# Kernel optimization log

Measured on AMD Instinct MI355X. Metric: run time of the kernel, lower is better.

The kernel has to match this reference:

```python
import jax, jax.numpy as jnp
import numpy as np

D = 1024      # hidden_size
H = 16        # num_heads
HD = D // H   # head_dim = 64
FF = 4096     # intermediate_size
DEPTH = 2
S = 2048      # packed sequence length
NSEG = 4     # number of image segments
EPS = 1e-6


def setup_inputs() -> dict:
    key = jax.random.key(0)
    ks = jax.random.split(key, 8)
    hidden_states = jax.random.normal(ks[0], (S, D), jnp.float32)
    cu_seqlens = jnp.arange(NSEG + 1, dtype=jnp.int32) * (S // NSEG)
    # rotary embedding like RiceRotaryEmbedding(head_dim//2): freqs of dim HD//4
    # per spatial axis, h/w concatenated -> HD//2, then duplicated -> HD
    inv_freq = 1.0 / (10000.0 ** (jnp.arange(0, HD // 2, 2, dtype=jnp.float32) / (HD // 2)))
    pos = jnp.arange(S, dtype=jnp.float32)
    freqs = jnp.outer(pos, inv_freq)                       # [S, HD//4]
    emb = jnp.concatenate([freqs] * 4, axis=-1)            # [S, HD]
    cos, sin = jnp.cos(emb), jnp.sin(emb)

    def w(k, shape, fan):
        return jax.random.normal(k, shape, jnp.float32) / np.sqrt(fan)

    return {
        "hidden_states": hidden_states,
        "cu_seqlens": cu_seqlens,
        "cos": cos,
        "sin": sin,
        "ln1_g": jnp.ones((DEPTH, D), jnp.float32),
        "ln1_b": jnp.zeros((DEPTH, D), jnp.float32),
        "qkv_w": w(ks[1], (DEPTH, D, 3 * D), D),
        "qkv_b": jnp.zeros((DEPTH, 3 * D), jnp.float32),
        "proj_w": w(ks[2], (DEPTH, D, D), D),
        "proj_b": jnp.zeros((DEPTH, D), jnp.float32),
        "ln2_g": jnp.ones((DEPTH, D), jnp.float32),
        "ln2_b": jnp.zeros((DEPTH, D), jnp.float32),
        "fc1_w": w(ks[3], (DEPTH, D, FF), D),
        "fc1_b": jnp.zeros((DEPTH, FF), jnp.float32),
        "fc2_w": w(ks[4], (DEPTH, FF, D), FF),
        "fc2_b": jnp.zeros((DEPTH, D), jnp.float32),
    }


def _ln(x, g, b):
    m = jnp.mean(x, axis=-1, keepdims=True)
    v = jnp.mean(jnp.square(x - m), axis=-1, keepdims=True)
    return (x - m) / jnp.sqrt(v + EPS) * g + b


def _rotate_half(x):
    x1, x2 = jnp.split(x, 2, axis=-1)
    return jnp.concatenate([-x2, x1], axis=-1)


def reference(hidden_states, cu_seqlens, cos, sin,
              ln1_g, ln1_b, qkv_w, qkv_b, proj_w, proj_b,
              ln2_g, ln2_b, fc1_w, fc1_b, fc2_w, fc2_b):
    S_, D_ = hidden_states.shape
    # segment id per token from cu_seqlens -> block-diagonal additive mask
    seg = jnp.searchsorted(cu_seqlens[1:], jnp.arange(S_, dtype=jnp.int32), side="right")
    neg = jnp.finfo(jnp.float32).min
    bias = jnp.where(seg[:, None] == seg[None, :], 0.0, neg)   # [S, S]
    cos_e = cos[:, None, :]  # broadcast over heads, [S,1,HD]
    sin_e = sin[:, None, :]
    scale = 1.0 / np.sqrt(HD)

    x = hidden_states
    for i in range(DEPTH):
        # --- attention ---
        h = _ln(x, ln1_g[i], ln1_b[i])
        qkv = h @ qkv_w[i] + qkv_b[i]                           # [S, 3D]
        q, k, v = [t.reshape(S_, H, HD) for t in jnp.split(qkv, 3, axis=-1)]
        q = q * cos_e + _rotate_half(q) * sin_e
        k = k * cos_e + _rotate_half(k) * sin_e
        scores = jnp.einsum("shd,thd->hst", q, k) * scale + bias  # [H,S,S]
        w_ = jax.nn.softmax(scores.astype(jnp.float32), axis=-1)
        ao = jnp.einsum("hst,thd->shd", w_, v).reshape(S_, D_)
        x = x + ao @ proj_w[i] + proj_b[i]
        # --- mlp ---
        h2 = _ln(x, ln2_g[i], ln2_b[i])
        x = x + jax.nn.gelu(h2 @ fc1_w[i] + fc1_b[i], approximate=False) @ fc2_w[i] + fc2_b[i]
    return x
```

## Files before the change

### kernel.cpp

```cpp
#include <hip/hip_runtime.h>
#include <hip/hip_bf16.h>
#include <math.h>

#define Dm 1024
#define Hn 16
#define HDm 64
#define FFm 4096
#define Sn 2048
#define SEG 512
#define EPSV 1e-6f

typedef __attribute__((ext_vector_type(4))) float f32x4;
typedef __attribute__((ext_vector_type(8))) short s16x8;
typedef __attribute__((ext_vector_type(4))) short s16x4;

__device__ inline short f2bf(float f) {
  __hip_bfloat16 h = __float2bfloat16(f);
  short s;
  __builtin_memcpy(&s, &h, 2);
  return s;
}
__device__ inline float bf2f(short s) {
  unsigned u = ((unsigned)(unsigned short)s) << 16;
  float f;
  __builtin_memcpy(&f, &u, 4);
  return f;
}

__device__ inline float wred_sum(float v) {
#pragma unroll
  for (int m = 32; m > 0; m >>= 1) v += __shfl_xor(v, m, 64);
  return v;
}

__device__ inline void gld16(const short* g, short* lds_base) {
  __builtin_amdgcn_global_load_lds(
      (const __attribute__((address_space(1))) void*)g,
      (__attribute__((address_space(3))) void*)lds_base, 16, 0, 0);
}

__global__ __launch_bounds__(256) void ln_kernel(const float* __restrict__ x,
                                                 const float* __restrict__ g,
                                                 const float* __restrict__ b,
                                                 short* __restrict__ out) {
  const int row = blockIdx.x;
  const int tid = threadIdx.x;
  f32x4 v = *reinterpret_cast<const f32x4*>(x + (size_t)row * Dm + tid * 4);
  float s1 = v.x + v.y + v.z + v.w;
  float s2 = v.x * v.x + v.y * v.y + v.z * v.z + v.w * v.w;
  s1 = wred_sum(s1);
  s2 = wred_sum(s2);
  __shared__ float t1[4], t2[4];
  if ((tid & 63) == 0) { t1[tid >> 6] = s1; t2[tid >> 6] = s2; }
  __syncthreads();
  s1 = t1[0] + t1[1] + t1[2] + t1[3];
  s2 = t2[0] + t2[1] + t2[2] + t2[3];
  const float mean = s1 * (1.0f / Dm);
  const float var = s2 * (1.0f / Dm) - mean * mean;
  const float rstd = rsqrtf(var + EPSV);
  f32x4 gv = *reinterpret_cast<const f32x4*>(g + tid * 4);
  f32x4 bv = *reinterpret_cast<const f32x4*>(b + tid * 4);
  s16x4 o;
#pragma unroll
  for (int j = 0; j < 4; ++j)
    o[j] = f2bf((v[j] - mean) * rstd * gv[j] + bv[j]);
  *reinterpret_cast<s16x4*>(out + (size_t)row * Dm + tid * 4) = o;
}

template <int SPLIT>
__global__ __launch_bounds__(256) void redln_bf(const short* __restrict__ pb,
                                                const float* __restrict__ bias,
                                                const float* __restrict__ res,
                                                const float* __restrict__ g,
                                                const float* __restrict__ b,
                                                float* __restrict__ xout,
                                                short* __restrict__ h) {
  const int row = blockIdx.x;
  const int tid = threadIdx.x;
  const size_t idx = (size_t)row * Dm + tid * 4;
  f32x4 o = *reinterpret_cast<const f32x4*>(res + idx);
  o += *reinterpret_cast<const f32x4*>(bias + tid * 4);
#pragma unroll
  for (int s = 0; s < SPLIT; ++s) {
    s16x4 v = *reinterpret_cast<const s16x4*>(pb + (size_t)s * Sn * Dm + idx);
#pragma unroll
    for (int j = 0; j < 4; ++j) o[j] += bf2f(v[j]);
  }
  *reinterpret_cast<f32x4*>(xout + idx) = o;
  float s1 = o.x + o.y + o.z + o.w;
  float s2 = o.x * o.x + o.y * o.y + o.z * o.z + o.w * o.w;
  s1 = wred_sum(s1);
  s2 = wred_sum(s2);
  __shared__ float t1[4], t2[4];
  if ((tid & 63) == 0) { t1[tid >> 6] = s1; t2[tid >> 6] = s2; }
  __syncthreads();
  s1 = t1[0] + t1[1] + t1[2] + t1[3];
  s2 = t2[0] + t2[1] + t2[2] + t2[3];
  const float mean = s1 * (1.0f / Dm);
  const float var = s2 * (1.0f / Dm) - mean * mean;
  const float rstd = rsqrtf(var + EPSV);
  f32x4 gv = *reinterpret_cast<const f32x4*>(g + tid * 4);
  f32x4 bv = *reinterpret_cast<const f32x4*>(b + tid * 4);
  s16x4 ho;
#pragma unroll
  for (int j = 0; j < 4; ++j)
    ho[j] = f2bf((o[j] - mean) * rstd * gv[j] + bv[j]);
  *reinterpret_cast<s16x4*>(h + idx) = ho;
}

template <int SPLIT>
__global__ __launch_bounds__(256) void fcred_bf(const short* __restrict__ pb,
                                                const float* __restrict__ bias,
                                                const float* __restrict__ res,
                                                float* __restrict__ out) {
  const size_t i = ((size_t)blockIdx.x * 256 + threadIdx.x) * 4;
  f32x4 o = *reinterpret_cast<const f32x4*>(res + i);
  o += *reinterpret_cast<const f32x4*>(bias + (i & (Dm - 1)));
#pragma unroll
  for (int s = 0; s < SPLIT; ++s) {
    s16x4 v = *reinterpret_cast<const s16x4*>(pb + (size_t)s * Sn * Dm + i);
#pragma unroll
    for (int j = 0; j < 4; ++j) o[j] += bf2f(v[j]);
  }
  *reinterpret_cast<f32x4*>(out + i) = o;
}

__global__ __launch_bounds__(256) void wt_kernel(const float* __restrict__ W,
                                                 short* __restrict__ Wt,
                                                 int K, int N, int ldw) {
  __shared__ float t[32][33];
  const int n0 = blockIdx.x * 32, k0 = blockIdx.y * 32;
  const int tx = threadIdx.x & 31, ty = threadIdx.x >> 5;
#pragma unroll
  for (int r = 0; r < 32; r += 8)
    t[r + ty][tx] = W[(size_t)(k0 + r + ty) * ldw + n0 + tx];
  __syncthreads();
#pragma unroll
  for (int r = 0; r < 32; r += 8)
    Wt[(size_t)(n0 + r + ty) * K + k0 + tx] = f2bf(t[tx][r + ty]);
}

__global__ __launch_bounds__(256) void wtb_kernel(const short* __restrict__ V,
                                                  short* __restrict__ Vt,
                                                  int K, int N, int ldv) {
  __shared__ short t[32][34];
  const int n0 = blockIdx.x * 32, k0 = blockIdx.y * 32;
  const int tx = threadIdx.x & 31, ty = threadIdx.x >> 5;
#pragma unroll
  for (int r = 0; r < 32; r += 8)
    t[r + ty][tx] = V[(size_t)(k0 + r + ty) * ldv + n0 + tx];
  __syncthreads();
#pragma unroll
  for (int r = 0; r < 32; r += 8)
    Vt[(size_t)(n0 + r + ty) * K + k0 + tx] = t[tx][r + ty];
}

__global__ __launch_bounds__(256, 2) void attn_kernel(const short* __restrict__ qkvb,
                                                      const short* __restrict__ vT,
                                                      short* __restrict__ ao) {
  __shared__ short Ps[4][16][520];
  const int tid = threadIdx.x;
  const int lane = tid & 63;
  const int wave = tid >> 6;
  const int l15 = lane & 15, lg = lane >> 4;
  const int z = blockIdx.x;
  const int qblk = blockIdx.y;
  const int seg = z & 3, head = z >> 2;
  const int qrow = seg * SEG + qblk * 64 + wave * 16;

  const short* Qg = qkvb + (size_t)(qrow + l15) * 3072 + head * HDm + lg * 8;
  s16x8 qf0 = *reinterpret_cast<const s16x8*>(Qg);
  s16x8 qf1 = *reinterpret_cast<const s16x8*>(Qg + 32);

  f32x4 acc[8][4] = {};
  const short* Kg = qkvb + (size_t)(seg * SEG + l15) * 3072 + Dm + head * HDm + lg * 8;
#pragma unroll
  for (int kt = 0; kt < 8; ++kt) {
#pragma unroll
    for (int fj = 0; fj < 4; ++fj) {
      const short* kp = Kg + (size_t)(kt * 64 + fj * 16) * 3072;
      s16x8 b0 = *reinterpret_cast<const s16x8*>(kp);
      s16x8 b1 = *reinterpret_cast<const s16x8*>(kp + 32);
      acc[kt][fj] = __builtin_amdgcn_mfma_f32_16x16x32_bf16(qf0, b0, acc[kt][fj], 0, 0, 0);
      acc[kt][fj] = __builtin_amdgcn_mfma_f32_16x16x32_bf16(qf1, b1, acc[kt][fj], 0, 0, 0);
    }
  }

  float mx[4], inv[4];
#pragma unroll
  for (int r = 0; r < 4; ++r) {
    float m = acc[0][0][r];
#pragma unroll
    for (int kt = 0; kt < 8; ++kt)
#pragma unroll
      for (int fj = 0; fj < 4; ++fj) m = fmaxf(m, acc[kt][fj][r]);
#pragma unroll
    for (int d = 1; d < 16; d <<= 1) m = fmaxf(m, __shfl_xor(m, d, 64));
    mx[r] = m * 0.125f;
  }
#pragma unroll
  for (int r = 0; r < 4; ++r) {
    float s = 0.f;
#pragma unroll
    for (int kt = 0; kt < 8; ++kt)
#pragma unroll
      for (int fj = 0; fj < 4; ++fj) {
        float pv = __expf(acc[kt][fj][r] * 0.125f - mx[r]);
        acc[kt][fj][r] = pv;
        s += pv;
      }
#pragma unroll
    for (int d = 1; d < 16; d <<= 1) s += __shfl_xor(s, d, 64);
    inv[r] = 1.0f / s;
  }

#pragma unroll
  for (int kt = 0; kt < 8; ++kt)
#pragma unroll
    for (int fj = 0; fj < 4; ++fj)
#pragma unroll
      for (int r = 0; r < 4; ++r)
        Ps[wave][lg * 4 + r][kt * 64 + fj * 16 + l15] = f2bf(acc[kt][fj][r]);
  asm volatile("s_waitcnt lgkmcnt(0)" ::: "memory");
  __builtin_amdgcn_sched_barrier(0);

  f32x4 pv[4] = {};
  const short* Vg = vT + (size_t)(head * HDm) * Sn + seg * SEG;
#pragma unroll
  for (int kt = 0; kt < 8; ++kt)
#pragma unroll
    for (int c = 0; c < 2; ++c) {
      s16x8 pa = *reinterpret_cast<const s16x8*>(
          &Ps[wave][l15][kt * 64 + c * 32 + lg * 8]);
#pragma unroll
      for (int fj = 0; fj < 4; ++fj) {
        s16x8 pb = *reinterpret_cast<const s16x8*>(
            Vg + (size_t)(fj * 16 + l15) * Sn + kt * 64 + c * 32 + lg * 8);
        pv[fj] = __builtin_amdgcn_mfma_f32_16x16x32_bf16(pa, pb, pv[fj], 0, 0, 0);
      }
    }

#pragma unroll
  for (int fj = 0; fj < 4; ++fj)
#pragma unroll
    for (int r = 0; r < 4; ++r)
      ao[(size_t)(qrow + lg * 4 + r) * Dm + head * HDm + fj * 16 + l15] =
          f2bf(pv[fj][r] * inv[r]);
}

struct GemmArgs {
  const short* A; int lda;
  const short* B; int ldb;
  void* C; int ldc;
  int M, N, K;
  const float* bias;
  const float* cosb; const float* sinb;
  float scale;
};

template <int BM, int BN, int SPLIT, int MODE>
__global__ __launch_bounds__(256) void gemm6(GemmArgs p) {
  constexpr int WN = 2;
  constexpr int WM = 2;
  constexpr int FI = BM / WM / 16;
  constexpr int FJ = BN / WN / 16;
  const int z = blockIdx.z;
  const short* A = p.A;
  const short* B = p.B;
  char* Cb = (char*)p.C;
  int kbase = 0, nkt = p.K >> 6;
  const int gx = gridDim.x;
  const int nwg = gx * gridDim.y;
  const int orig = blockIdx.y * gx + blockIdx.x;
  const int sid = (orig & 7) * (nwg >> 3) + (orig >> 3);
  const int tileM = (sid / gx) * BM;
  const int tileN = (sid % gx) * BN;
  if (MODE == 3 || MODE == 6) {
    kbase = z * (p.K / SPLIT);
    nkt = (p.K / SPLIT) >> 6;
    Cb += (size_t)z * p.M * p.N * ((MODE == 3) ? 4 : 2);
  }
  __shared__ short As[BM * 64];
  __shared__ short Bs[BN * 64];
  const int tid = threadIdx.x;
  const int lane = tid & 63;
  const int wave = tid >> 6;
  const int l15 = lane & 15;
  const int lg = lane >> 4;
  const int rx = l15 & 7;
  const int wr = (wave / WN) * (BM / WM);
  const int wc = (wave % WN) * (BN / WN);
  const int srow = lane >> 3;
  const int scol = ((lane & 7) ^ srow) * 8;

  f32x4 acc[FI][FJ] = {};

  const short* Ag = A + (size_t)(tileM + wave * 8 + srow) * p.lda + scol + kbase;
  const short* Bg = B + (size_t)(tileN + wave * 8 + srow) * p.ldb + scol + kbase;

  for (int kt = 0; kt < nkt; ++kt) {
    const int k0 = kt * 64;
#pragma unroll
    for (int j = 0; j < BM / 32; ++j)
      gld16(Ag + (size_t)(j * 32) * p.lda + k0, &As[(j * 32 + wave * 8) * 64]);
#pragma unroll
    for (int j = 0; j < BN / 32; ++j)
      gld16(Bg + (size_t)(j * 32) * p.ldb + k0, &Bs[(j * 32 + wave * 8) * 64]);
    __syncthreads();
#pragma unroll
    for (int kk = 0; kk < 64; kk += 32) {
      const int kkc = kk >> 3;
      s16x8 af[FI], bfr[FJ];
#pragma unroll
      for (int f = 0; f < FI; ++f)
        af[f] = *reinterpret_cast<const s16x8*>(
            &As[(wr + f * 16 + l15) * 64 + (((lg + kkc) ^ rx) << 3)]);
#pragma unroll
      for (int f = 0; f < FJ; ++f)
        bfr[f] = *reinterpret_cast<const s16x8*>(
            &Bs[(wc + f * 16 + l15) * 64 + (((lg + kkc) ^ rx) << 3)]);
#pragma unroll
      for (int fi = 0; fi < FI; ++fi)
#pragma unroll
        for (int fj = 0; fj < FJ; ++fj)
          acc[fi][fj] = __builtin_amdgcn_mfma_f32_16x16x32_bf16(
              af[fi], bfr[fj], acc[fi][fj], 0, 0, 0);
    }
    __syncthreads();
  }

  if (MODE == 4) {
    short* Cs = (short*)Cb;
    const bool isqk = (tileN + wc) < 2048;
#pragma unroll
    for (int fi = 0; fi < FI; ++fi) {
#pragma unroll
      for (int fj = 0; fj < FJ; ++fj) {
#pragma unroll
        for (int r = 0; r < 4; ++r) {
          const int row = tileM + wr + fi * 16 + lg * 4 + r;
          const int col = tileN + wc + fj * 16 + l15;
          float a0 = acc[fi][fj][r] + p.bias[col];
          float vout;
          if (isqk) {
            float a1 = acc[fi][fj ^ 2][r] + p.bias[col ^ 32];
            const int dl = fj * 16 + l15;
            const float c = p.cosb[(size_t)row * HDm + dl];
            const float sn = p.sinb[(size_t)row * HDm + dl];
            vout = (fj < 2) ? (a0 * c - a1 * sn) : (a0 * c + a1 * sn);
          } else {
            vout = a0;
          }
          Cs[(size_t)row * p.ldc + col] = f2bf(vout);
        }
      }
    }
    return;
  }

#pragma unroll
  for (int fi = 0; fi < FI; ++fi) {
#pragma unroll
    for (int fj = 0; fj < FJ; ++fj) {
#pragma unroll
      for (int r = 0; r < 4; ++r) {
        const int row = tileM + wr + fi * 16 + lg * 4 + r;
        const int col = tileN + wc + fj * 16 + l15;
        float v = acc[fi][fj][r] * p.scale;
        if (MODE == 5) {
          v += p.bias[col];
          v = 0.5f * v * (1.0f + erff(v * 0.70710678118654752f));
        }
        if (MODE == 5 || MODE == 6)
          reinterpret_cast<short*>(Cb)[(size_t)row * p.ldc + col] = f2bf(v);
        else
          reinterpret_cast<float*>(Cb)[(size_t)row * p.ldc + col] = v;
      }
    }
  }
}

extern "C" void kernel_launch(void* const* d_in, const int* in_sizes, int n_in,
                              void* d_out, int out_size, void* d_ws, size_t ws_size,
                              hipStream_t stream) {
  const float* x0 = (const float*)d_in[0];
  const float* cosb = (const float*)d_in[2];
  const float* sinb = (const float*)d_in[3];
  const float* ln1_g = (const float*)d_in[4];
  const float* ln1_b = (const float*)d_in[5];
  const float* qkv_w = (const float*)d_in[6];
  const float* qkv_b = (const float*)d_in[7];
  const float* proj_w = (const float*)d_in[8];
  const float* proj_b = (const float*)d_in[9];
  const float* ln2_g = (const float*)d_in[10];
  const float* ln2_b = (const float*)d_in[11];
  const float* fc1_w = (const float*)d_in[12];
  const float* fc1_b = (const float*)d_in[13];
  const float* fc2_w = (const float*)d_in[14];
  const float* fc2_b = (const float*)d_in[15];

  char* ws = (char*)d_ws;
  size_t off = 0;
  auto alloc = [&](size_t bytes) {
    void* p = ws + off;
    off += (bytes + 255) & ~(size_t)255;
    return p;
  };
  short* wqkvT = (short*)alloc((size_t)2 * 3072 * 1024 * 2);
  short* wprojT = (short*)alloc((size_t)2 * 1024 * 1024 * 2);
  short* wfc1T = (short*)alloc((size_t)2 * 4096 * 1024 * 2);
  short* wfc2T = (short*)alloc((size_t)2 * 1024 * 4096 * 2);
  float* xbuf = (float*)alloc((size_t)Sn * Dm * 4);
  short* hbuf = (short*)alloc((size_t)Sn * Dm * 2);
  short* qkvb = (short*)alloc((size_t)Sn * 3 * Dm * 2);
  float* pbuf = (float*)alloc((size_t)4 * Sn * Dm * 4);
  short* pbufS = (short*)pbuf;
  short* ao = (short*)alloc((size_t)Sn * Dm * 2);
  short* ffn = (short*)alloc((size_t)Sn * FFm * 2);
  short* vT = ffn;
  (void)ws_size; (void)in_sizes; (void)n_in; (void)out_size;

  for (int i = 0; i < 2; ++i) {
    wt_kernel<<<dim3(96, 32), 256, 0, stream>>>(
        qkv_w + (size_t)i * Dm * 3072, wqkvT + (size_t)i * 3072 * Dm, Dm, 3072, 3072);
    wt_kernel<<<dim3(32, 32), 256, 0, stream>>>(
        proj_w + (size_t)i * Dm * Dm, wprojT + (size_t)i * Dm * Dm, Dm, Dm, Dm);
    wt_kernel<<<dim3(128, 32), 256, 0, stream>>>(
        fc1_w + (size_t)i * Dm * FFm, wfc1T + (size_t)i * FFm * Dm, Dm, FFm, FFm);
    wt_kernel<<<dim3(32, 128), 256, 0, stream>>>(
        fc2_w + (size_t)i * FFm * Dm, wfc2T + (size_t)i * Dm * FFm, FFm, Dm, Dm);
  }

  ln_kernel<<<dim3(Sn), 256, 0, stream>>>(x0, ln1_g, ln1_b, hbuf);

  for (int i = 0; i < 2; ++i) {
    const float* xin = i ? (const float*)xbuf : x0;

    {
      GemmArgs p = {};
      p.A = hbuf; p.lda = Dm;
      p.B = wqkvT + (size_t)i * 3072 * Dm; p.ldb = Dm;
      p.C = qkvb; p.ldc = 3 * Dm;
      p.M = Sn; p.N = 3 * Dm; p.K = Dm;
      p.bias = qkv_b + i * 3 * Dm; p.cosb = cosb; p.sinb = sinb; p.scale = 1.0f;
      gemm6<64, 128, 1, 4><<<dim3(24, 32, 1), 256, 0, stream>>>(p);
    }

    wtb_kernel<<<dim3(32, 64), 256, 0, stream>>>(qkvb + 2 * Dm, vT, Sn, Dm, 3 * Dm);

    attn_kernel<<<dim3(64, 8), 256, 0, stream>>>(qkvb, vT, ao);

    {
      GemmArgs p = {};
      p.A = ao; p.lda = Dm;
      p.B = wprojT + (size_t)i * Dm * Dm; p.ldb = Dm;
      p.C = pbufS; p.ldc = Dm;
      p.M = Sn; p.N = Dm; p.K = Dm; p.scale = 1.0f;
      gemm6<64, 64, 2, 6><<<dim3(16, 32, 2), 256, 0, stream>>>(p);
    }
    redln_bf<2><<<dim3(Sn), 256, 0, stream>>>(
        pbufS, proj_b + i * Dm, xin, ln2_g + i * Dm, ln2_b + i * Dm, xbuf, hbuf);

    {
      GemmArgs p = {};
      p.A = hbuf; p.lda = Dm;
      p.B = wfc1T + (size_t)i * FFm * Dm; p.ldb = Dm;
      p.C = ffn; p.ldc = FFm;
      p.M = Sn; p.N = FFm; p.K = Dm;
      p.bias = fc1_b + i * FFm; p.scale = 1.0f;
      gemm6<64, 128, 1, 5><<<dim3(32, 32, 1), 256, 0, stream>>>(p);
    }

    {
      GemmArgs p = {};
      p.A = ffn; p.lda = FFm;
      p.B = wfc2T + (size_t)i * Dm * FFm; p.ldb = FFm;
      p.C = pbufS; p.ldc = Dm;
      p.M = Sn; p.N = Dm; p.K = FFm; p.scale = 1.0f;
      gemm6<64, 128, 4, 6><<<dim3(8, 32, 4), 256, 0, stream>>>(p);
    }
    if (i == 0) {
      redln_bf<4><<<dim3(Sn), 256, 0, stream>>>(
          pbufS, fc2_b, xbuf, ln1_g + Dm, ln1_b + Dm, xbuf, hbuf);
    } else {
      fcred_bf<4><<<dim3(Sn * Dm / 1024), 256, 0, stream>>>(
          pbufS, fc2_b + Dm, xbuf, (float*)d_out);
    }
  }
}
```

Measured before the change: 326.1 us.

## Stage K tile in LDS for attention and batch weight transposes into one launch

The attention kernel now loads the whole 512x64 K block of a segment/head into swizzled shared memory with async global-to-LDS loads. It then reads K fragments from LDS instead of issuing strided global loads per wave, and reuses the same buffer for the swizzled P tile. The grid is reordered so the query blocks of one head/segment are adjacent, and s_setprio wraps the MFMA loops. The eight weight-transpose launches are merged into one job-table kernel, and dead scale and fp32 output paths are removed from the GEMM.

Measured after the change: 297.4 us. 1.1x faster.

```diff
diff --git a/kernel.cpp b/kernel.cpp
--- a/kernel.cpp
+++ b/kernel.cpp
@@ -125,15 +125,28 @@
   *reinterpret_cast<f32x4*>(out + i) = o;
 }
 
-__global__ __launch_bounds__(256) void wt_kernel(const float* __restrict__ W,
-                                                 short* __restrict__ Wt,
-                                                 int K, int N, int ldw) {
+struct WtJobs {
+  const float* src[8];
+  short* dst[8];
+  int K[8], N[8], start[9];
+};
+__global__ __launch_bounds__(256) void wtall_kernel(WtJobs jb) {
   __shared__ float t[32][33];
-  const int n0 = blockIdx.x * 32, k0 = blockIdx.y * 32;
+  const int bid = blockIdx.x;
+  int j = 0;
+#pragma unroll
+  for (int q = 1; q < 8; ++q)
+    if (bid >= jb.start[q]) j = q;
+  const int local = bid - jb.start[j];
+  const int K = jb.K[j], N = jb.N[j];
+  const int nx = N >> 5;
+  const int n0 = (local % nx) * 32, k0 = (local / nx) * 32;
+  const float* W = jb.src[j];
+  short* Wt = jb.dst[j];
   const int tx = threadIdx.x & 31, ty = threadIdx.x >> 5;
 #pragma unroll
   for (int r = 0; r < 32; r += 8)
-    t[r + ty][tx] = W[(size_t)(k0 + r + ty) * ldw + n0 + tx];
+    t[r + ty][tx] = W[(size_t)(k0 + r + ty) * N + n0 + tx];
   __syncthreads();
 #pragma unroll
   for (int r = 0; r < 32; r += 8)
@@ -155,36 +168,51 @@
     Vt[(size_t)(n0 + r + ty) * K + k0 + tx] = t[tx][r + ty];
 }
 
-__global__ __launch_bounds__(256, 2) void attn_kernel(const short* __restrict__ qkvb,
-                                                      const short* __restrict__ vT,
-                                                      short* __restrict__ ao) {
-  __shared__ short Ps[4][16][520];
+__global__ __launch_bounds__(256, 2) void attn2_kernel(const short* __restrict__ qkvb,
+                                                       const short* __restrict__ vT,
+                                                       short* __restrict__ ao) {
+  __shared__ short Ks[512 * 64];
   const int tid = threadIdx.x;
   const int lane = tid & 63;
   const int wave = tid >> 6;
-  const int l15 = lane & 15, lg = lane >> 4;
-  const int z = blockIdx.x;
-  const int qblk = blockIdx.y;
+  const int l15 = lane & 15, lg = lane >> 4, rx = l15 & 7;
+  const int qblk = blockIdx.x;
+  const int z = blockIdx.y;
   const int seg = z & 3, head = z >> 2;
-  const int qrow = seg * SEG + qblk * 64 + wave * 16;
-
-  const short* Qg = qkvb + (size_t)(qrow + l15) * 3072 + head * HDm + lg * 8;
+  const int qbase = seg * SEG + qblk * 64 + wave * 16;
+
+  const int srow = tid >> 3;
+  const int sch = ((tid & 7) ^ (srow & 7)) * 8;
+  const short* Kg = qkvb + (size_t)(seg * SEG + srow) * 3072 + Dm +
+                    head * HDm + sch;
+#pragma unroll
+  for (int j = 0; j < 16; ++j)
+    gld16(Kg + (size_t)(j * 32) * 3072, &Ks[(j * 32 + wave * 8) * 64]);
+
+  const short* Qg = qkvb + (size_t)(qbase + l15) * 3072 + head * HDm + lg * 8;
   s16x8 qf0 = *reinterpret_cast<const s16x8*>(Qg);
   s16x8 qf1 = *reinterpret_cast<const s16x8*>(Qg + 32);
 
+  asm volatile("s_waitcnt vmcnt(0)" ::: "memory");
+  __builtin_amdgcn_s_barrier();
+  __builtin_amdgcn_sched_barrier(0);
+
   f32x4 acc[8][4] = {};
-  const short* Kg = qkvb + (size_t)(seg * SEG + l15) * 3072 + Dm + head * HDm + lg * 8;
+  __builtin_amdgcn_s_setprio(1);
 #pragma unroll
   for (int kt = 0; kt < 8; ++kt) {
 #pragma unroll
     for (int fj = 0; fj < 4; ++fj) {
-      const short* kp = Kg + (size_t)(kt * 64 + fj * 16) * 3072;
-      s16x8 b0 = *reinterpret_cast<const s16x8*>(kp);
-      s16x8 b1 = *reinterpret_cast<const s16x8*>(kp + 32);
+      const int R = kt * 64 + fj * 16 + l15;
+      s16x8 b0 = *reinterpret_cast<const s16x8*>(
+          &Ks[R * 64 + ((lg ^ rx) << 3)]);
+      s16x8 b1 = *reinterpret_cast<const s16x8*>(
+          &Ks[R * 64 + (((lg + 4) ^ rx) << 3)]);
       acc[kt][fj] = __builtin_amdgcn_mfma_f32_16x16x32_bf16(qf0, b0, acc[kt][fj], 0, 0, 0);
       acc[kt][fj] = __builtin_amdgcn_mfma_f32_16x16x32_bf16(qf1, b1, acc[kt][fj], 0, 0, 0);
     }
   }
+  __builtin_amdgcn_s_setprio(0);
 
   float mx[4], inv[4];
 #pragma unroll
@@ -214,37 +242,46 @@
     inv[r] = 1.0f / s;
   }
 
+  __syncthreads();
+
+  short* Psw = Ks + wave * 16 * 512;
 #pragma unroll
   for (int kt = 0; kt < 8; ++kt)
 #pragma unroll
     for (int fj = 0; fj < 4; ++fj)
 #pragma unroll
-      for (int r = 0; r < 4; ++r)
-        Ps[wave][lg * 4 + r][kt * 64 + fj * 16 + l15] = f2bf(acc[kt][fj][r]);
+      for (int r = 0; r < 4; ++r) {
+        const int q = lg * 4 + r;
+        const int k = kt * 64 + fj * 16 + l15;
+        const int c = k >> 3;
+        const int cs = (c & ~7) | ((c & 7) ^ (q & 7));
+        Psw[q * 512 + cs * 8 + (k & 7)] = f2bf(acc[kt][fj][r]);
+      }
   asm volatile("s_waitcnt lgkmcnt(0)" ::: "memory");
   __builtin_amdgcn_sched_barrier(0);
 
   f32x4 pv[4] = {};
   const short* Vg = vT + (size_t)(head * HDm) * Sn + seg * SEG;
-#pragma unroll
-  for (int kt = 0; kt < 8; ++kt)
-#pragma unroll
-    for (int c = 0; c < 2; ++c) {
-      s16x8 pa = *reinterpret_cast<const s16x8*>(
-          &Ps[wave][l15][kt * 64 + c * 32 + lg * 8]);
-#pragma unroll
-      for (int fj = 0; fj < 4; ++fj) {
-        s16x8 pb = *reinterpret_cast<const s16x8*>(
-            Vg + (size_t)(fj * 16 + l15) * Sn + kt * 64 + c * 32 + lg * 8);
-        pv[fj] = __builtin_amdgcn_mfma_f32_16x16x32_bf16(pa, pb, pv[fj], 0, 0, 0);
-      }
-    }
+  __builtin_amdgcn_s_setprio(1);
+#pragma unroll
+  for (int ks = 0; ks < 16; ++ks) {
+    const int ca = ks * 4 + lg;
+    const int csa = (ca & ~7) | ((ca & 7) ^ rx);
+    s16x8 pa = *reinterpret_cast<const s16x8*>(&Psw[l15 * 512 + csa * 8]);
+#pragma unroll
+    for (int fj = 0; fj < 4; ++fj) {
+      s16x8 pb = *reinterpret_cast<const s16x8*>(
+          Vg + (size_t)(fj * 16 + l15) * Sn + ks * 32 + lg * 8);
+      pv[fj] = __builtin_amdgcn_mfma_f32_16x16x32_bf16(pa, pb, pv[fj], 0, 0, 0);
+    }
+  }
+  __builtin_amdgcn_s_setprio(0);
 
 #pragma unroll
   for (int fj = 0; fj < 4; ++fj)
 #pragma unroll
     for (int r = 0; r < 4; ++r)
-      ao[(size_t)(qrow + lg * 4 + r) * Dm + head * HDm + fj * 16 + l15] =
+      ao[(size_t)(qbase + lg * 4 + r) * Dm + head * HDm + fj * 16 + l15] =
           f2bf(pv[fj][r] * inv[r]);
 }
 
@@ -275,10 +312,10 @@
   const int sid = (orig & 7) * (nwg >> 3) + (orig >> 3);
   const int tileM = (sid / gx) * BM;
   const int tileN = (sid % gx) * BN;
-  if (MODE == 3 || MODE == 6) {
+  if (MODE == 6) {
     kbase = z * (p.K / SPLIT);
     nkt = (p.K / SPLIT) >> 6;
-    Cb += (size_t)z * p.M * p.N * ((MODE == 3) ? 4 : 2);
+    Cb += (size_t)z * p.M * p.N * 2;
   }
   __shared__ short As[BM * 64];
   __shared__ short Bs[BN * 64];
@@ -366,15 +403,12 @@
       for (int r = 0; r < 4; ++r) {
         const int row = tileM + wr + fi * 16 + lg * 4 + r;
         const int col = tileN + wc + fj * 16 + l15;
-        float v = acc[fi][fj][r] * p.scale;
+        float v = acc[fi][fj][r];
         if (MODE == 5) {
           v += p.bias[col];
           v = 0.5f * v * (1.0f + erff(v * 0.70710678118654752f));
         }
-        if (MODE == 5 || MODE == 6)
-          reinterpret_cast<short*>(Cb)[(size_t)row * p.ldc + col] = f2bf(v);
-        else
-          reinterpret_cast<float*>(Cb)[(size_t)row * p.ldc + col] = v;
+        reinterpret_cast<short*>(Cb)[(size_t)row * p.ldc + col] = f2bf(v);
       }
     }
   }
@@ -420,15 +454,30 @@
   short* vT = ffn;
   (void)ws_size; (void)in_sizes; (void)n_in; (void)out_size;
 
-  for (int i = 0; i < 2; ++i) {
-    wt_kernel<<<dim3(96, 32), 256, 0, stream>>>(
-        qkv_w + (size_t)i * Dm * 3072, wqkvT + (size_t)i * 3072 * Dm, Dm, 3072, 3072);
-    wt_kernel<<<dim3(32, 32), 256, 0, stream>>>(
-        proj_w + (size_t)i * Dm * Dm, wprojT + (size_t)i * Dm * Dm, Dm, Dm, Dm);
-    wt_kernel<<<dim3(128, 32), 256, 0, stream>>>(
-        fc1_w + (size_t)i * Dm * FFm, wfc1T + (size_t)i * FFm * Dm, Dm, FFm, FFm);
-    wt_kernel<<<dim3(32, 128), 256, 0, stream>>>(
-        fc2_w + (size_t)i * FFm * Dm, wfc2T + (size_t)i * Dm * FFm, FFm, Dm, Dm);
+  {
+    WtJobs jb;
+    int acc = 0;
+    for (int i = 0; i < 2; ++i) {
+      const int base = i * 4;
+      jb.src[base + 0] = qkv_w + (size_t)i * Dm * 3072;
+      jb.dst[base + 0] = wqkvT + (size_t)i * 3072 * Dm;
+      jb.K[base + 0] = Dm; jb.N[base + 0] = 3072;
+      jb.src[base + 1] = proj_w + (size_t)i * Dm * Dm;
+      jb.dst[base + 1] = wprojT + (size_t)i * Dm * Dm;
+      jb.K[base + 1] = Dm; jb.N[base + 1] = Dm;
+      jb.src[base + 2] = fc1_w + (size_t)i * Dm * FFm;
+      jb.dst[base + 2] = wfc1T + (size_t)i * FFm * Dm;
+      jb.K[base + 2] = Dm; jb.N[base + 2] = FFm;
+      jb.src[base + 3] = fc2_w + (size_t)i * FFm * Dm;
+      jb.dst[base + 3] = wfc2T + (size_t)i * Dm * FFm;
+      jb.K[base + 3] = FFm; jb.N[base + 3] = Dm;
+    }
+    for (int j = 0; j < 8; ++j) {
+      jb.start[j] = acc;
+      acc += (jb.N[j] >> 5) * (jb.K[j] >> 5);
+    }
+    jb.start[8] = acc;
+    wtall_kernel<<<dim3(acc), 256, 0, stream>>>(jb);
   }
 
   ln_kernel<<<dim3(Sn), 256, 0, stream>>>(x0, ln1_g, ln1_b, hbuf);
@@ -442,20 +491,20 @@
       p.B = wqkvT + (size_t)i * 3072 * Dm; p.ldb = Dm;
       p.C = qkvb; p.ldc = 3 * Dm;
       p.M = Sn; p.N = 3 * Dm; p.K = Dm;
-      p.bias = qkv_b + i * 3 * Dm; p.cosb = cosb; p.sinb = sinb; p.scale = 1.0f;
+      p.bias = qkv_b + i * 3 * Dm; p.cosb = cosb; p.sinb = sinb;
       gemm6<64, 128, 1, 4><<<dim3(24, 32, 1), 256, 0, stream>>>(p);
     }
 
     wtb_kernel<<<dim3(32, 64), 256, 0, stream>>>(qkvb + 2 * Dm, vT, Sn, Dm, 3 * Dm);
 
-    attn_kernel<<<dim3(64, 8), 256, 0, stream>>>(qkvb, vT, ao);
+    attn2_kernel<<<dim3(8, 64), 256, 0, stream>>>(qkvb, vT, ao);
 
     {
       GemmArgs p = {};
       p.A = ao; p.lda = Dm;
       p.B = wprojT + (size_t)i * Dm * Dm; p.ldb = Dm;
       p.C = pbufS; p.ldc = Dm;
-      p.M = Sn; p.N = Dm; p.K = Dm; p.scale = 1.0f;
+      p.M = Sn; p.N = Dm; p.K = Dm;
       gemm6<64, 64, 2, 6><<<dim3(16, 32, 2), 256, 0, stream>>>(p);
     }
     redln_bf<2><<<dim3(Sn), 256, 0, stream>>>(
@@ -467,7 +516,7 @@
       p.B = wfc1T + (size_t)i * FFm * Dm; p.ldb = Dm;
       p.C = ffn; p.ldc = FFm;
       p.M = Sn; p.N = FFm; p.K = Dm;
-      p.bias = fc1_b + i * FFm; p.scale = 1.0f;
+      p.bias = fc1_b + i * FFm;
       gemm6<64, 128, 1, 5><<<dim3(32, 32, 1), 256, 0, stream>>>(p);
     }
 
@@ -476,7 +525,7 @@
       p.A = ffn; p.lda = FFm;
       p.B = wfc2T + (size_t)i * Dm * FFm; p.ldb = FFm;
       p.C = pbufS; p.ldc = Dm;
-      p.M = Sn; p.N = Dm; p.K = FFm; p.scale = 1.0f;
+      p.M = Sn; p.N = Dm; p.K = FFm;
       gemm6<64, 128, 4, 6><<<dim3(8, 32, 4), 256, 0, stream>>>(p);
     }
     if (i == 0) {
```
